# Performance work log

Measured on AMD Instinct MI355X. Metric: run time of the kernel, lower is better.

Reference implementation:

```python
import jax, jax.numpy as jnp
import numpy as np
import math

QUERY_DIM = 128
SCALE = 1.0 / math.sqrt(QUERY_DIM)

def setup_inputs() -> dict:
    key = jax.random.key(0)
    k1, k2, k3 = jax.random.split(key, 3)
    B, Q, K, D = 16, 2048, 2048, 128
    return {
        "query": jax.random.normal(k1, (B, Q, D), dtype=jnp.float32),
        "keys": jax.random.normal(k2, (B, K, D), dtype=jnp.float32),
        "values": jax.random.normal(k3, (B, K, D), dtype=jnp.float32),
    }

def reference(query, keys, values):
    # energy[b,q,k] = sum_d query[b,q,d] * keys[b,k,d], scaled then softmax over k
    energy = jnp.einsum("bqd,bkd->bqk", query, keys) * SCALE
    attn = jax.nn.softmax(energy, axis=2)
    # linear combination over values
    return jnp.einsum("bqk,bkv->bqv", attn, values)
```

## Files before the change

kernel.cpp:

```cpp
#include <hip/hip_runtime.h>
#include <hip/hip_bf16.h>


#define BATCH 16
#define QLEN 2048
#define KLEN 2048
#define DIM 128
#define BM 64
#define BN 64
#define NT (KLEN / BN)

#define VBYTES 16384
#define SMEM_BYTES 34048

typedef __attribute__((ext_vector_type(8))) short bf16x8;
typedef __attribute__((ext_vector_type(4))) float f32x4;

__device__ __forceinline__ short f2bf(float x) {
    union { float f; unsigned u; } v; v.f = x;
    unsigned r = v.u + 0x7FFFu + ((v.u >> 16) & 1u);
    return (short)(r >> 16);
}
__device__ __forceinline__ unsigned pkbf(float a, float b) {
    union { float f; unsigned u; } x, y; x.f = a; y.f = b;
    unsigned ra = x.u + 0x7FFFu + ((x.u >> 16) & 1u);
    unsigned rb = y.u + 0x7FFFu + ((y.u >> 16) & 1u);
    return __builtin_amdgcn_perm(rb, ra, 0x07060302u);
}
__device__ __forceinline__ float fexp2(float x) {
#if __has_builtin(__builtin_amdgcn_exp2f)
    return __builtin_amdgcn_exp2f(x);
#else
    return exp2f(x);
#endif
}

#define GLOAD_LDS16(g, l) \
    __builtin_amdgcn_global_load_lds((__attribute__((address_space(1))) void*)(g), \
                                     (__attribute__((address_space(3))) void*)(l), 16, 0, 0)

#define TSTR 72
__global__ __launch_bounds__(256) void prepass_kernel(
    const float* __restrict__ kg, const float* __restrict__ vg,
    unsigned short* __restrict__ Kws, unsigned short* __restrict__ Vtws)
{
    __shared__ unsigned short T[DIM * TSTR];
    const int tid = threadIdx.x;
    const int kb  = blockIdx.x * BN;
    const int b   = blockIdx.y;
    const float* kt = kg + ((size_t)b * KLEN + kb) * DIM;
    const float* vt = vg + ((size_t)b * KLEN + kb) * DIM;

    unsigned short* koF = Kws + ((size_t)b * KLEN + kb) * DIM;
#pragma unroll
    for (int j = 0; j < 4; ++j) {
        int o  = tid + 256 * j;
        int s  = o >> 6;
        int l  = o & 63;
        int qd = l >> 4;
        int lm_ = l & 15;
        int kh   = s >> 3;
        int dk   = (s >> 1) & 3;
        int half = s & 1;
        int r   = kh * 32 + half * 16 + lm_;
        int key = (r & 3) | ((r & 4) << 1) | ((r & 8) << 1) | ((r & 16) >> 2) | (r & 32);
        const float* src = kt + key * DIM + dk * 32 + qd * 8;
        float4 k0 = *(const float4*)(src);
        float4 k1 = *(const float4*)(src + 4);
        uint4 w;
        w.x = pkbf(k0.x, k0.y); w.y = pkbf(k0.z, k0.w);
        w.z = pkbf(k1.x, k1.y); w.w = pkbf(k1.z, k1.w);
        *(uint4*)(koF + o * 8) = w;
    }

#pragma unroll
    for (int j = 0; j < 8; ++j) {
        int idx = tid + 256 * j;
        int key = idx >> 5;
        int d4  = (idx & 31) * 4;
        float4 vv = *(const float4*)(vt + key * DIM + d4);
        T[(d4 + 0) * TSTR + key] = (unsigned short)f2bf(vv.x);
        T[(d4 + 1) * TSTR + key] = (unsigned short)f2bf(vv.y);
        T[(d4 + 2) * TSTR + key] = (unsigned short)f2bf(vv.z);
        T[(d4 + 3) * TSTR + key] = (unsigned short)f2bf(vv.w);
    }
    __syncthreads();
    unsigned short* vo = Vtws + (size_t)b * DIM * KLEN + kb;
#pragma unroll
    for (int j = 0; j < 4; ++j) {
        int c = tid + 256 * j;
        int d = c >> 3;
        int g = c & 7;
        uint4 u = *(const uint4*)&T[d * TSTR + g * 8];
        *(uint4*)(vo + (size_t)d * KLEN + g * 8) = u;
    }
}

__global__ __launch_bounds__(256, 2) void attn_flash_kernel(
    const float* __restrict__ qg,
    const unsigned short* __restrict__ Kws,
    const unsigned short* __restrict__ Vtws,
    float* __restrict__ outg)
{
    __shared__ __align__(16) char SMC[SMEM_BYTES];

    const int tid  = threadIdx.x;
    const int wave = tid >> 6;
    const int lane = tid & 63;
    const int lm   = lane & 15;
    const int quad = lane >> 4;
    const int rw   = wave >> 1;
    const int kw   = wave & 1;

    const int n  = blockIdx.y * gridDim.x + blockIdx.x;
    const int np = (n & 7) * 64 + (n >> 3);
    const int b     = np >> 5;
    const int qbase = (np & 31) * BM + rw * 32;

    const float QSCALE = 0.08838834764831845f * 1.4426950408889634f;

    bf16x8 qfA[4], qfB[4];
    {
        const float* qrowA = qg + (size_t)(b * QLEN + qbase + lm) * DIM;
        const float* qrowB = qrowA + 16 * DIM;
#pragma unroll
        for (int dk = 0; dk < 4; ++dk) {
            int d0 = dk * 32 + quad * 8;
            float4 a = *(const float4*)(qrowA + d0);
            float4 c = *(const float4*)(qrowA + d0 + 4);
            uint4 u;
            u.x = pkbf(a.x*QSCALE, a.y*QSCALE); u.y = pkbf(a.z*QSCALE, a.w*QSCALE);
            u.z = pkbf(c.x*QSCALE, c.y*QSCALE); u.w = pkbf(c.z*QSCALE, c.w*QSCALE);
            qfA[dk] = *(bf16x8*)&u;
            float4 e = *(const float4*)(qrowB + d0);
            float4 g = *(const float4*)(qrowB + d0 + 4);
            uint4 v;
            v.x = pkbf(e.x*QSCALE, e.y*QSCALE); v.y = pkbf(e.z*QSCALE, e.w*QSCALE);
            v.z = pkbf(g.x*QSCALE, g.y*QSCALE); v.w = pkbf(g.z*QSCALE, g.w*QSCALE);
            qfB[dk] = *(bf16x8*)&v;
        }
    }

    f32x4 OA[8], OB[8];
#pragma unroll
    for (int i = 0; i < 8; ++i) { OA[i] = 0.0f; OB[i] = 0.0f; }
    float lrA = 0.f, lrB = 0.f;

    const unsigned short* kfp = Kws + (size_t)b * KLEN * DIM
                              + kw * 4096 + lane * 8;

    const unsigned short* Vtb = Vtws + (size_t)b * DIM * KLEN;
    const char* vdma[4];
    {
        int gv  = lane & 7;
        int d0v = wave * 32 + (lane >> 3);
#pragma unroll
        for (int i = 0; i < 4; ++i) {
            int dv = d0v + 8 * i;
            vdma[i] = (const char*)Vtb + (size_t)dv * (KLEN * 2) + ((gv ^ (dv & 7)) << 4);
        }
    }

    const int vfo = lm * 128 + (((kw * 4 + quad) ^ (lm & 7)) << 4);

    auto dma = [&](int tt, int bb) {
        char* ldsV = SMC + bb * VBYTES + wave * 4096;
        size_t vo = (size_t)tt * 128;
#pragma unroll
        for (int i = 0; i < 4; ++i)
            GLOAD_LDS16(vdma[i] + vo, ldsV + i * 1024);
    };

    f32x4 SP0a, SP1a, SP0b, SP1b;
    bf16x8 vp[8];
    bf16x8 kp[8];

#pragma unroll
    for (int i = 0; i < 8; ++i) kp[i] = *(const bf16x8*)(kfp + i * 512);
    dma(0, 0);
    __syncthreads();
    {
        dma(1, 1);
        f32x4 S0a = 0.0f, S1a = 0.0f, S0b = 0.0f, S1b = 0.0f;
#pragma unroll
        for (int dk = 0; dk < 4; ++dk) {
            S0a = __builtin_amdgcn_mfma_f32_16x16x32_bf16(kp[2*dk],   qfA[dk], S0a, 0, 0, 0);
            S0b = __builtin_amdgcn_mfma_f32_16x16x32_bf16(kp[2*dk],   qfB[dk], S0b, 0, 0, 0);
            S1a = __builtin_amdgcn_mfma_f32_16x16x32_bf16(kp[2*dk+1], qfA[dk], S1a, 0, 0, 0);
            S1b = __builtin_amdgcn_mfma_f32_16x16x32_bf16(kp[2*dk+1], qfB[dk], S1b, 0, 0, 0);
        }
        const char* bufV = SMC;
#pragma unroll
        for (int dt = 0; dt < 8; ++dt)
            vp[dt] = *(const bf16x8*)(bufV + vfo + dt * 2048);
#pragma unroll
        for (int i = 0; i < 8; ++i)
            kp[i] = *(const bf16x8*)(kfp + 8192 + i * 512);
        SP0a = S0a; SP1a = S1a; SP0b = S0b; SP1b = S1b;
    }
    __syncthreads();

    for (int t = 1; t < NT; ++t) {
        if (t + 1 < NT) dma(t + 1, (t + 1) & 1);

        float a0 = fexp2(SP0a[0]), a1 = fexp2(SP0a[1]), a2 = fexp2(SP0a[2]), a3 = fexp2(SP0a[3]);
        float a4 = fexp2(SP1a[0]), a5 = fexp2(SP1a[1]), a6 = fexp2(SP1a[2]), a7 = fexp2(SP1a[3]);
        float b0 = fexp2(SP0b[0]), b1 = fexp2(SP0b[1]), b2 = fexp2(SP0b[2]), b3 = fexp2(SP0b[3]);
        float b4 = fexp2(SP1b[0]), b5 = fexp2(SP1b[1]), b6 = fexp2(SP1b[2]), b7 = fexp2(SP1b[3]);
        uint4 puA, puB;
        puA.x = pkbf(a0,a1); puA.y = pkbf(a2,a3); puA.z = pkbf(a4,a5); puA.w = pkbf(a6,a7);
        puB.x = pkbf(b0,b1); puB.y = pkbf(b2,b3); puB.z = pkbf(b4,b5); puB.w = pkbf(b6,b7);
        bf16x8 pfA = *(bf16x8*)&puA;
        bf16x8 pfB = *(bf16x8*)&puB;
        lrA += ((a0+a1)+(a2+a3)) + ((a4+a5)+(a6+a7));
        lrB += ((b0+b1)+(b2+b3)) + ((b4+b5)+(b6+b7));

        f32x4 S0a = 0.0f, S1a = 0.0f, S0b = 0.0f, S1b = 0.0f;
#pragma unroll
        for (int dk = 0; dk < 4; ++dk) {
            S0a = __builtin_amdgcn_mfma_f32_16x16x32_bf16(kp[2*dk],   qfA[dk], S0a, 0, 0, 0);
            S0b = __builtin_amdgcn_mfma_f32_16x16x32_bf16(kp[2*dk],   qfB[dk], S0b, 0, 0, 0);
            S1a = __builtin_amdgcn_mfma_f32_16x16x32_bf16(kp[2*dk+1], qfA[dk], S1a, 0, 0, 0);
            S1b = __builtin_amdgcn_mfma_f32_16x16x32_bf16(kp[2*dk+1], qfB[dk], S1b, 0, 0, 0);
        }

        if (t + 1 < NT) {
            const unsigned short* kt1 = kfp + (size_t)(t + 1) * 8192;
#pragma unroll
            for (int i = 0; i < 8; ++i)
                kp[i] = *(const bf16x8*)(kt1 + i * 512);
        }

#pragma unroll
        for (int dt = 0; dt < 8; ++dt) {
            OA[dt] = __builtin_amdgcn_mfma_f32_16x16x32_bf16(vp[dt], pfA, OA[dt], 0, 0, 0);
            OB[dt] = __builtin_amdgcn_mfma_f32_16x16x32_bf16(vp[dt], pfB, OB[dt], 0, 0, 0);
        }

        {
            const char* bufV = SMC + (t & 1) * VBYTES;
#pragma unroll
            for (int dt = 0; dt < 8; ++dt)
                vp[dt] = *(const bf16x8*)(bufV + vfo + dt * 2048);
        }

        SP0a = S0a; SP1a = S1a; SP0b = S0b; SP1b = S1b;

        __syncthreads();
    }

    {
        float a0 = fexp2(SP0a[0]), a1 = fexp2(SP0a[1]), a2 = fexp2(SP0a[2]), a3 = fexp2(SP0a[3]);
        float a4 = fexp2(SP1a[0]), a5 = fexp2(SP1a[1]), a6 = fexp2(SP1a[2]), a7 = fexp2(SP1a[3]);
        float b0 = fexp2(SP0b[0]), b1 = fexp2(SP0b[1]), b2 = fexp2(SP0b[2]), b3 = fexp2(SP0b[3]);
        float b4 = fexp2(SP1b[0]), b5 = fexp2(SP1b[1]), b6 = fexp2(SP1b[2]), b7 = fexp2(SP1b[3]);
        uint4 puA, puB;
        puA.x = pkbf(a0,a1); puA.y = pkbf(a2,a3); puA.z = pkbf(a4,a5); puA.w = pkbf(a6,a7);
        puB.x = pkbf(b0,b1); puB.y = pkbf(b2,b3); puB.z = pkbf(b4,b5); puB.w = pkbf(b6,b7);
        bf16x8 pfA = *(bf16x8*)&puA;
        bf16x8 pfB = *(bf16x8*)&puB;
        lrA += ((a0+a1)+(a2+a3)) + ((a4+a5)+(a6+a7));
        lrB += ((b0+b1)+(b2+b3)) + ((b4+b5)+(b6+b7));
#pragma unroll
        for (int dt = 0; dt < 8; ++dt) {
            OA[dt] = __builtin_amdgcn_mfma_f32_16x16x32_bf16(vp[dt], pfA, OA[dt], 0, 0, 0);
            OB[dt] = __builtin_amdgcn_mfma_f32_16x16x32_bf16(vp[dt], pfB, OB[dt], 0, 0, 0);
        }
    }

    lrA += __shfl_xor(lrA, 16, 64); lrA += __shfl_xor(lrA, 32, 64);
    lrB += __shfl_xor(lrB, 16, 64); lrB += __shfl_xor(lrB, 32, 64);

    float* Orw = (float*)SMC + rw * 4256;
    if (kw == 1) {
#pragma unroll
        for (int dt = 0; dt < 8; ++dt) {
            *(f32x4*)&Orw[lm*132        + dt*16 + quad*4] = OA[dt];
            *(f32x4*)&Orw[(16+lm)*132   + dt*16 + quad*4] = OB[dt];
        }
        if (lane < 16)      Orw[4224 + lm]      = lrA;
        else if (lane < 32) Orw[4224 + 16 + lm] = lrB;
    }
    __syncthreads();
    if (kw == 0) {
        float invA = 1.0f / (lrA + Orw[4224 + lm]);
        float invB = 1.0f / (lrB + Orw[4224 + 16 + lm]);
        float* orowA = outg + (size_t)(b * QLEN + qbase + lm) * DIM;
        float* orowB = orowA + 16 * DIM;
#pragma unroll
        for (int dt = 0; dt < 8; ++dt) {
            f32x4 oA = *(const f32x4*)&Orw[lm*132      + dt*16 + quad*4];
            f32x4 oB = *(const f32x4*)&Orw[(16+lm)*132 + dt*16 + quad*4];
            *(f32x4*)&orowA[dt*16 + quad*4] = (OA[dt] + oA) * invA;
            *(f32x4*)&orowB[dt*16 + quad*4] = (OB[dt] + oB) * invB;
        }
    }
}

extern "C" void kernel_launch(void* const* d_in, const int* in_sizes, int n_in,
                              void* d_out, int out_size, void* d_ws, size_t ws_size,
                              hipStream_t stream) {
    const float* q = (const float*)d_in[0];
    const float* k = (const float*)d_in[1];
    const float* v = (const float*)d_in[2];
    float* o = (float*)d_out;
    unsigned short* Kws  = (unsigned short*)d_ws;
    unsigned short* Vtws = Kws + (size_t)BATCH * KLEN * DIM;
    dim3 grid(KLEN / BN, BATCH);
    prepass_kernel<<<grid, 256, 0, stream>>>(k, v, Kws, Vtws);
    dim3 grid2(QLEN / BM, BATCH);
    attn_flash_kernel<<<grid2, 256, 0, stream>>>(q, Kws, Vtws, o);
}
```

Measured before the change: 130.4 us.

## Switch attention MFMAs from 16x16x32 to 32x32x16 bf16 tiles

Replaces the 16x16x32 bf16 MFMA tiling with 32x32x16 MFMAs for both the QK^T and PV products. The K prepass layout, Q fragment loading, V LDS read offsets and output epilogue are all remapped to the 32-lane fragment layout. Larger MFMA tiles issue fewer instructions per tile and read fewer operands per flop. The trade-offs are longer per-instruction latency that the schedule must hide, and a more complex element-to-row mapping in the epilogue.

```diff
diff --git a/kernel.cpp b/kernel.cpp
--- a/kernel.cpp
+++ b/kernel.cpp
@@ -15,6 +15,7 @@
 
 typedef __attribute__((ext_vector_type(8))) short bf16x8;
 typedef __attribute__((ext_vector_type(4))) float f32x4;
+typedef __attribute__((ext_vector_type(16))) float f32x16;
 
 __device__ __forceinline__ short f2bf(float x) {
     union { float f; unsigned u; } v; v.f = x;
@@ -55,16 +56,14 @@
 #pragma unroll
     for (int j = 0; j < 4; ++j) {
         int o  = tid + 256 * j;
-        int s  = o >> 6;
+        int st = o >> 6;
         int l  = o & 63;
-        int qd = l >> 4;
-        int lm_ = l & 15;
-        int kh   = s >> 3;
-        int dk   = (s >> 1) & 3;
-        int half = s & 1;
-        int r   = kh * 32 + half * 16 + lm_;
-        int key = (r & 3) | ((r & 4) << 1) | ((r & 8) << 1) | ((r & 16) >> 2) | (r & 32);
-        const float* src = kt + key * DIM + dk * 32 + qd * 8;
+        int h  = l >> 5;
+        int v  = l & 31;
+        int kw_ = st >> 3;
+        int s   = st & 7;
+        int key = kw_ * 32 + ((v & 19) | ((v & 8) >> 1) | ((v & 4) << 1));
+        const float* src = kt + key * DIM + 16 * s + 8 * h;
         float4 k0 = *(const float4*)(src);
         float4 k1 = *(const float4*)(src + 4);
         uint4 w;
@@ -107,8 +106,8 @@
     const int tid  = threadIdx.x;
     const int wave = tid >> 6;
     const int lane = tid & 63;
-    const int lm   = lane & 15;
-    const int quad = lane >> 4;
+    const int ln   = lane & 31;
+    const int h    = lane >> 5;
     const int rw   = wave >> 1;
     const int kw   = wave & 1;
 
@@ -119,32 +118,25 @@
 
     const float QSCALE = 0.08838834764831845f * 1.4426950408889634f;
 
-    bf16x8 qfA[4], qfB[4];
+    bf16x8 qf[8];
     {
-        const float* qrowA = qg + (size_t)(b * QLEN + qbase + lm) * DIM;
-        const float* qrowB = qrowA + 16 * DIM;
-#pragma unroll
-        for (int dk = 0; dk < 4; ++dk) {
-            int d0 = dk * 32 + quad * 8;
-            float4 a = *(const float4*)(qrowA + d0);
-            float4 c = *(const float4*)(qrowA + d0 + 4);
+        const float* qrow = qg + (size_t)(b * QLEN + qbase + ln) * DIM;
+#pragma unroll
+        for (int s = 0; s < 8; ++s) {
+            int d0 = 16 * s + 8 * h;
+            float4 a = *(const float4*)(qrow + d0);
+            float4 c = *(const float4*)(qrow + d0 + 4);
             uint4 u;
             u.x = pkbf(a.x*QSCALE, a.y*QSCALE); u.y = pkbf(a.z*QSCALE, a.w*QSCALE);
             u.z = pkbf(c.x*QSCALE, c.y*QSCALE); u.w = pkbf(c.z*QSCALE, c.w*QSCALE);
-            qfA[dk] = *(bf16x8*)&u;
-            float4 e = *(const float4*)(qrowB + d0);
-            float4 g = *(const float4*)(qrowB + d0 + 4);
-            uint4 v;
-            v.x = pkbf(e.x*QSCALE, e.y*QSCALE); v.y = pkbf(e.z*QSCALE, e.w*QSCALE);
-            v.z = pkbf(g.x*QSCALE, g.y*QSCALE); v.w = pkbf(g.z*QSCALE, g.w*QSCALE);
-            qfB[dk] = *(bf16x8*)&v;
-        }
-    }
-
-    f32x4 OA[8], OB[8];
-#pragma unroll
-    for (int i = 0; i < 8; ++i) { OA[i] = 0.0f; OB[i] = 0.0f; }
-    float lrA = 0.f, lrB = 0.f;
+            qf[s] = *(bf16x8*)&u;
+        }
+    }
+
+    f32x16 O[4];
+#pragma unroll
+    for (int i = 0; i < 4; ++i) O[i] = 0.0f;
+    float lr = 0.f;
 
     const unsigned short* kfp = Kws + (size_t)b * KLEN * DIM
                               + kw * 4096 + lane * 8;
@@ -161,7 +153,12 @@
         }
     }
 
-    const int vfo = lm * 128 + (((kw * 4 + quad) ^ (lm & 7)) << 4);
+    int vro[8];
+#pragma unroll
+    for (int i = 0; i < 8; ++i) {
+        int db = i >> 1, ks = i & 1;
+        vro[i] = (32 * db + ln) * 128 + (((kw * 4 + ks * 2 + h) ^ (ln & 7)) << 4);
+    }
 
     auto dma = [&](int tt, int bb) {
         char* ldsV = SMC + bb * VBYTES + wave * 4096;
@@ -171,129 +168,124 @@
             GLOAD_LDS16(vdma[i] + vo, ldsV + i * 1024);
     };
 
-    f32x4 SP0a, SP1a, SP0b, SP1b;
+    f32x16 SP;
     bf16x8 vp[8];
     bf16x8 kp[8];
 
 #pragma unroll
-    for (int i = 0; i < 8; ++i) kp[i] = *(const bf16x8*)(kfp + i * 512);
+    for (int s = 0; s < 8; ++s) kp[s] = *(const bf16x8*)(kfp + s * 512);
     dma(0, 0);
     __syncthreads();
     {
         dma(1, 1);
-        f32x4 S0a = 0.0f, S1a = 0.0f, S0b = 0.0f, S1b = 0.0f;
-#pragma unroll
-        for (int dk = 0; dk < 4; ++dk) {
-            S0a = __builtin_amdgcn_mfma_f32_16x16x32_bf16(kp[2*dk],   qfA[dk], S0a, 0, 0, 0);
-            S0b = __builtin_amdgcn_mfma_f32_16x16x32_bf16(kp[2*dk],   qfB[dk], S0b, 0, 0, 0);
-            S1a = __builtin_amdgcn_mfma_f32_16x16x32_bf16(kp[2*dk+1], qfA[dk], S1a, 0, 0, 0);
-            S1b = __builtin_amdgcn_mfma_f32_16x16x32_bf16(kp[2*dk+1], qfB[dk], S1b, 0, 0, 0);
-        }
+        f32x16 S = 0.0f;
+#pragma unroll
+        for (int s = 0; s < 8; ++s)
+            S = __builtin_amdgcn_mfma_f32_32x32x16_bf16(kp[s], qf[s], S, 0, 0, 0);
         const char* bufV = SMC;
 #pragma unroll
-        for (int dt = 0; dt < 8; ++dt)
-            vp[dt] = *(const bf16x8*)(bufV + vfo + dt * 2048);
-#pragma unroll
         for (int i = 0; i < 8; ++i)
-            kp[i] = *(const bf16x8*)(kfp + 8192 + i * 512);
-        SP0a = S0a; SP1a = S1a; SP0b = S0b; SP1b = S1b;
+            vp[i] = *(const bf16x8*)(bufV + vro[i]);
+#pragma unroll
+        for (int s = 0; s < 8; ++s)
+            kp[s] = *(const bf16x8*)(kfp + 8192 + s * 512);
+        SP = S;
     }
     __syncthreads();
 
     for (int t = 1; t < NT; ++t) {
         if (t + 1 < NT) dma(t + 1, (t + 1) & 1);
 
-        float a0 = fexp2(SP0a[0]), a1 = fexp2(SP0a[1]), a2 = fexp2(SP0a[2]), a3 = fexp2(SP0a[3]);
-        float a4 = fexp2(SP1a[0]), a5 = fexp2(SP1a[1]), a6 = fexp2(SP1a[2]), a7 = fexp2(SP1a[3]);
-        float b0 = fexp2(SP0b[0]), b1 = fexp2(SP0b[1]), b2 = fexp2(SP0b[2]), b3 = fexp2(SP0b[3]);
-        float b4 = fexp2(SP1b[0]), b5 = fexp2(SP1b[1]), b6 = fexp2(SP1b[2]), b7 = fexp2(SP1b[3]);
-        uint4 puA, puB;
-        puA.x = pkbf(a0,a1); puA.y = pkbf(a2,a3); puA.z = pkbf(a4,a5); puA.w = pkbf(a6,a7);
-        puB.x = pkbf(b0,b1); puB.y = pkbf(b2,b3); puB.z = pkbf(b4,b5); puB.w = pkbf(b6,b7);
-        bf16x8 pfA = *(bf16x8*)&puA;
-        bf16x8 pfB = *(bf16x8*)&puB;
-        lrA += ((a0+a1)+(a2+a3)) + ((a4+a5)+(a6+a7));
-        lrB += ((b0+b1)+(b2+b3)) + ((b4+b5)+(b6+b7));
-
-        f32x4 S0a = 0.0f, S1a = 0.0f, S0b = 0.0f, S1b = 0.0f;
-#pragma unroll
-        for (int dk = 0; dk < 4; ++dk) {
-            S0a = __builtin_amdgcn_mfma_f32_16x16x32_bf16(kp[2*dk],   qfA[dk], S0a, 0, 0, 0);
-            S0b = __builtin_amdgcn_mfma_f32_16x16x32_bf16(kp[2*dk],   qfB[dk], S0b, 0, 0, 0);
-            S1a = __builtin_amdgcn_mfma_f32_16x16x32_bf16(kp[2*dk+1], qfA[dk], S1a, 0, 0, 0);
-            S1b = __builtin_amdgcn_mfma_f32_16x16x32_bf16(kp[2*dk+1], qfB[dk], S1b, 0, 0, 0);
-        }
+        float p0 = fexp2(SP[0]),  p1 = fexp2(SP[1]),  p2 = fexp2(SP[2]),  p3 = fexp2(SP[3]);
+        float p4 = fexp2(SP[4]),  p5 = fexp2(SP[5]),  p6 = fexp2(SP[6]),  p7 = fexp2(SP[7]);
+        float p8 = fexp2(SP[8]),  p9 = fexp2(SP[9]),  pa = fexp2(SP[10]), pb = fexp2(SP[11]);
+        float pc = fexp2(SP[12]), pd = fexp2(SP[13]), pe = fexp2(SP[14]), pf_ = fexp2(SP[15]);
+        uint4 pu0, pu1;
+        pu0.x = pkbf(p0,p1); pu0.y = pkbf(p2,p3); pu0.z = pkbf(p4,p5); pu0.w = pkbf(p6,p7);
+        pu1.x = pkbf(p8,p9); pu1.y = pkbf(pa,pb); pu1.z = pkbf(pc,pd); pu1.w = pkbf(pe,pf_);
+        bf16x8 pf0 = *(bf16x8*)&pu0;
+        bf16x8 pf1 = *(bf16x8*)&pu1;
+        lr += (((p0+p1)+(p2+p3)) + ((p4+p5)+(p6+p7)))
+            + (((p8+p9)+(pa+pb)) + ((pc+pd)+(pe+pf_)));
+
+        f32x16 S = 0.0f;
+#pragma unroll
+        for (int s = 0; s < 8; ++s)
+            S = __builtin_amdgcn_mfma_f32_32x32x16_bf16(kp[s], qf[s], S, 0, 0, 0);
 
         if (t + 1 < NT) {
             const unsigned short* kt1 = kfp + (size_t)(t + 1) * 8192;
 #pragma unroll
-            for (int i = 0; i < 8; ++i)
-                kp[i] = *(const bf16x8*)(kt1 + i * 512);
-        }
-
-#pragma unroll
-        for (int dt = 0; dt < 8; ++dt) {
-            OA[dt] = __builtin_amdgcn_mfma_f32_16x16x32_bf16(vp[dt], pfA, OA[dt], 0, 0, 0);
-            OB[dt] = __builtin_amdgcn_mfma_f32_16x16x32_bf16(vp[dt], pfB, OB[dt], 0, 0, 0);
+            for (int s = 0; s < 8; ++s)
+                kp[s] = *(const bf16x8*)(kt1 + s * 512);
+        }
+
+#pragma unroll
+        for (int db = 0; db < 4; ++db) {
+            O[db] = __builtin_amdgcn_mfma_f32_32x32x16_bf16(vp[db*2+0], pf0, O[db], 0, 0, 0);
+            O[db] = __builtin_amdgcn_mfma_f32_32x32x16_bf16(vp[db*2+1], pf1, O[db], 0, 0, 0);
         }
 
         {
             const char* bufV = SMC + (t & 1) * VBYTES;
 #pragma unroll
-            for (int dt = 0; dt < 8; ++dt)
-                vp[dt] = *(const bf16x8*)(bufV + vfo + dt * 2048);
-        }
-
-        SP0a = S0a; SP1a = S1a; SP0b = S0b; SP1b = S1b;
+            for (int i = 0; i < 8; ++i)
+                vp[i] = *(const bf16x8*)(bufV + vro[i]);
+        }
+
+        SP = S;
 
         __syncthreads();
     }
 
     {
-        float a0 = fexp2(SP0a[0]), a1 = fexp2(SP0a[1]), a2 = fexp2(SP0a[2]), a3 = fexp2(SP0a[3]);
-        float a4 = fexp2(SP1a[0]), a5 = fexp2(SP1a[1]), a6 = fexp2(SP1a[2]), a7 = fexp2(SP1a[3]);
-        float b0 = fexp2(SP0b[0]), b1 = fexp2(SP0b[1]), b2 = fexp2(SP0b[2]), b3 = fexp2(SP0b[3]);
-        float b4 = fexp2(SP1b[0]), b5 = fexp2(SP1b[1]), b6 = fexp2(SP1b[2]), b7 = fexp2(SP1b[3]);
-        uint4 puA, puB;
-        puA.x = pkbf(a0,a1); puA.y = pkbf(a2,a3); puA.z = pkbf(a4,a5); puA.w = pkbf(a6,a7);
-        puB.x = pkbf(b0,b1); puB.y = pkbf(b2,b3); puB.z = pkbf(b4,b5); puB.w = pkbf(b6,b7);
-        bf16x8 pfA = *(bf16x8*)&puA;
-        bf16x8 pfB = *(bf16x8*)&puB;
-        lrA += ((a0+a1)+(a2+a3)) + ((a4+a5)+(a6+a7));
-        lrB += ((b0+b1)+(b2+b3)) + ((b4+b5)+(b6+b7));
-#pragma unroll
-        for (int dt = 0; dt < 8; ++dt) {
-            OA[dt] = __builtin_amdgcn_mfma_f32_16x16x32_bf16(vp[dt], pfA, OA[dt], 0, 0, 0);
-            OB[dt] = __builtin_amdgcn_mfma_f32_16x16x32_bf16(vp[dt], pfB, OB[dt], 0, 0, 0);
-        }
-    }
-
-    lrA += __shfl_xor(lrA, 16, 64); lrA += __shfl_xor(lrA, 32, 64);
-    lrB += __shfl_xor(lrB, 16, 64); lrB += __shfl_xor(lrB, 32, 64);
+        float p0 = fexp2(SP[0]),  p1 = fexp2(SP[1]),  p2 = fexp2(SP[2]),  p3 = fexp2(SP[3]);
+        float p4 = fexp2(SP[4]),  p5 = fexp2(SP[5]),  p6 = fexp2(SP[6]),  p7 = fexp2(SP[7]);
+        float p8 = fexp2(SP[8]),  p9 = fexp2(SP[9]),  pa = fexp2(SP[10]), pb = fexp2(SP[11]);
+        float pc = fexp2(SP[12]), pd = fexp2(SP[13]), pe = fexp2(SP[14]), pf_ = fexp2(SP[15]);
+        uint4 pu0, pu1;
+        pu0.x = pkbf(p0,p1); pu0.y = pkbf(p2,p3); pu0.z = pkbf(p4,p5); pu0.w = pkbf(p6,p7);
+        pu1.x = pkbf(p8,p9); pu1.y = pkbf(pa,pb); pu1.z = pkbf(pc,pd); pu1.w = pkbf(pe,pf_);
+        bf16x8 pf0 = *(bf16x8*)&pu0;
+        bf16x8 pf1 = *(bf16x8*)&pu1;
+        lr += (((p0+p1)+(p2+p3)) + ((p4+p5)+(p6+p7)))
+            + (((p8+p9)+(pa+pb)) + ((pc+pd)+(pe+pf_)));
+#pragma unroll
+        for (int db = 0; db < 4; ++db) {
+            O[db] = __builtin_amdgcn_mfma_f32_32x32x16_bf16(vp[db*2+0], pf0, O[db], 0, 0, 0);
+            O[db] = __builtin_amdgcn_mfma_f32_32x32x16_bf16(vp[db*2+1], pf1, O[db], 0, 0, 0);
+        }
+    }
+
+    lr += __shfl_xor(lr, 32, 64);
 
     float* Orw = (float*)SMC + rw * 4256;
     if (kw == 1) {
 #pragma unroll
-        for (int dt = 0; dt < 8; ++dt) {
-            *(f32x4*)&Orw[lm*132        + dt*16 + quad*4] = OA[dt];
-            *(f32x4*)&Orw[(16+lm)*132   + dt*16 + quad*4] = OB[dt];
-        }
-        if (lane < 16)      Orw[4224 + lm]      = lrA;
-        else if (lane < 32) Orw[4224 + 16 + lm] = lrB;
+        for (int db = 0; db < 4; ++db)
+#pragma unroll
+            for (int c = 0; c < 4; ++c) {
+                f32x4 ov;
+                ov[0] = O[db][4*c+0]; ov[1] = O[db][4*c+1];
+                ov[2] = O[db][4*c+2]; ov[3] = O[db][4*c+3];
+                *(f32x4*)&Orw[ln * 132 + 32*db + 8*c + 4*h] = ov;
+            }
+        if (lane < 32) Orw[4224 + ln] = lr;
     }
     __syncthreads();
     if (kw == 0) {
-        float invA = 1.0f / (lrA + Orw[4224 + lm]);
-        float invB = 1.0f / (lrB + Orw[4224 + 16 + lm]);
-        float* orowA = outg + (size_t)(b * QLEN + qbase + lm) * DIM;
-        float* orowB = orowA + 16 * DIM;
-#pragma unroll
-        for (int dt = 0; dt < 8; ++dt) {
-            f32x4 oA = *(const f32x4*)&Orw[lm*132      + dt*16 + quad*4];
-            f32x4 oB = *(const f32x4*)&Orw[(16+lm)*132 + dt*16 + quad*4];
-            *(f32x4*)&orowA[dt*16 + quad*4] = (OA[dt] + oA) * invA;
-            *(f32x4*)&orowB[dt*16 + quad*4] = (OB[dt] + oB) * invB;
-        }
+        float inv = 1.0f / (lr + Orw[4224 + ln]);
+        float* orow = outg + (size_t)(b * QLEN + qbase + ln) * DIM;
+#pragma unroll
+        for (int db = 0; db < 4; ++db)
+#pragma unroll
+            for (int c = 0; c < 4; ++c) {
+                f32x4 ov;
+                ov[0] = O[db][4*c+0]; ov[1] = O[db][4*c+1];
+                ov[2] = O[db][4*c+2]; ov[3] = O[db][4*c+3];
+                f32x4 om = *(const f32x4*)&Orw[ln * 132 + 32*db + 8*c + 4*h];
+                *(f32x4*)&orow[32*db + 8*c + 4*h] = (ov + om) * inv;
+            }
     }
 }
 
```

New measurement: 134.9 us. 3.4% more time.
